# Performance work log

Hardware: AMD Instinct MI355X
Metric: run time of the kernel (lower is better)

## Reference

```python
import jax, jax.numpy as jnp
import numpy as np

NS = 16384   # N*S support examples
NQ = 16384   # N*Q query examples
D = 64       # embedding dim
N_CLASSES = 64


def setup_inputs() -> dict:
    key = jax.random.key(0)
    k1, k2, k3 = jax.random.split(key, 3)
    support_embeddings = jax.random.normal(k1, (NS, D), dtype=jnp.float32)
    query_embeddings = jax.random.normal(k2, (NQ, D), dtype=jnp.float32)
    labels = jax.random.randint(k3, (NS,), 0, N_CLASSES)
    support_labels_onehot = jax.nn.one_hot(labels, N_CLASSES, dtype=jnp.float32)
    return {
        "support_embeddings": support_embeddings,
        "query_embeddings": query_embeddings,
        "support_labels_onehot": support_labels_onehot,
    }


def reference(support_embeddings, query_embeddings, support_labels_onehot):
    # Pairwise L2 distance via ||q||^2 + ||s||^2 - 2 q.s (same math as
    # tf.norm(q[:,None,:] - s[None,:,:], axis=2) without the [NQ,NS,D] blowup).
    sq_s = jnp.sum(support_embeddings * support_embeddings, axis=-1)  # [NS]
    sq_q = jnp.sum(query_embeddings * query_embeddings, axis=-1)      # [NQ]
    cross = jnp.einsum('qd,sd->qs', query_embeddings, support_embeddings)  # [NQ,NS]
    d2 = sq_q[:, None] + sq_s[None, :] - 2.0 * cross
    distance = jnp.sqrt(jnp.maximum(d2, 0.0))
    # top_k(-distance, k=1) == first argmin along support axis
    indices = jnp.argmin(distance, axis=1)                 # [NQ]
    labels_x = jnp.argmax(support_labels_onehot, axis=1)   # [NS]
    labels_pred = labels_x[indices]                        # [NQ] gather
    num_classes = support_labels_onehot.shape[1]
    labels_prob = jax.nn.one_hot(labels_pred, num_classes, dtype=support_labels_onehot.dtype)
    return labels_prob
```

## Files before the change

kernel.cpp:

```cpp
#include <hip/hip_runtime.h>


#define NTOT   16384
#define DIM    64
#define EPS_COEF 0.004f
#define EPS_ABS  0.05f
#define CINIT_COEF (-0.499f)
#define FLT_BIG 3.4e38f

typedef __attribute__((ext_vector_type(8))) short short8;
typedef __attribute__((ext_vector_type(4))) float float4v;

__device__ __forceinline__ ushort f16_bits(float x) {
  union { _Float16 f; ushort u; } c;
  c.f = (_Float16)x;
  return c.u;
}

__device__ __forceinline__ void pin8(short8& v) {
  asm volatile("" : "+v"(v));
}

__global__ __launch_bounds__(256) void k_prep(
    const float* __restrict__ S, const float* __restrict__ Q,
    ushort* __restrict__ Sh, ushort* __restrict__ Qh,
    float* __restrict__ sqS, float* __restrict__ sqQ,
    float* __restrict__ sqSc, float* __restrict__ S_T) {
  __shared__ float tile[64][65];
  const int tid = threadIdx.x;
  const bool isS = blockIdx.x < 256;
  const int rbase = (blockIdx.x & 255) * 64;
  const float* __restrict__ src = isS ? S : Q;
  ushort* __restrict__ dh = isS ? Sh : Qh;

  const int tx = tid & 63;
  const int ty = tid >> 6;
#pragma unroll
  for (int i = 0; i < 16; ++i) {
    const int r = i * 4 + ty;
    tile[r][tx] = src[(size_t)(rbase + r) * DIM + tx];
  }
  __syncthreads();

  if (isS) {
#pragma unroll
    for (int i = 0; i < 16; ++i) {
      const int d = i * 4 + ty;
      S_T[(size_t)d * NTOT + rbase + tx] = tile[tx][d];
    }
  }

  const int panel = tid >> 6;
  const int half = (tid >> 5) & 1;
  const int slot0 = (tid & 31) * 2;
#pragma unroll
  for (int ss = 0; ss < 2; ++ss) {
    const int s = slot0 + ss;
    const int m = s & 15;
    const int q8 = s >> 4;
    const int row = panel * 16 + m;
    const int kb = half * 32 + q8 * 8;
    short8 hv;
#pragma unroll
    for (int j = 0; j < 8; ++j) hv[j] = (short)f16_bits(tile[row][kb + j]);
    const size_t goff =
        (size_t)((rbase >> 4) + panel) * 1024 + (size_t)half * 512 + (size_t)s * 8;
    *(short8*)&dh[goff] = hv;
  }

  if (tid < 64) {
    float acc = 0.0f;
#pragma unroll
    for (int d = 0; d < DIM; ++d) {
      const float v = tile[tid][d];
      acc = fmaf(v, v, acc);
    }
    if (isS) {
      sqS[rbase + tid] = acc;
      sqSc[rbase + tid] = CINIT_COEF * acc;
    } else {
      sqQ[rbase + tid] = acc;
    }
  }
}


#define MFMA16F(A, B, C) __builtin_amdgcn_mfma_f32_16x16x32_f16(A, B, C, 0, 0, 0)

template <int BST>
__global__ __launch_bounds__(256, 4) void k_phaseA(
    const ushort* __restrict__ Sh, const ushort* __restrict__ Qh,
    const float* __restrict__ sqSc, float* __restrict__ bmin) {
  constexpr int NSB = NTOT / (16 * BST);
  constexpr int SBLK = 16 * BST;
  __shared__ ushort spanel[2][4096];
  __shared__ float ssq[2][64];

  const int tid = threadIdx.x;
  const int l = tid & 63;
  const int w = tid >> 6;
  const int lm = l & 15;
  const int lq = l >> 4;
  const int split = blockIdx.x;
  const int qbase = blockIdx.y * 256 + w * 64;
  const int sbase = split * 512;

  short8 qh[4][2];
#pragma unroll
  for (int t = 0; t < 4; ++t) {
    const size_t pb = (size_t)((qbase >> 4) + t) * 1024 + (size_t)l * 8;
    qh[t][0] = *(const short8*)&Qh[pb];
    qh[t][1] = *(const short8*)&Qh[pb + 512];
  }
#pragma unroll
  for (int t = 0; t < 4; ++t) {
    pin8(qh[t][0]);
    pin8(qh[t][1]);
  }

  auto stage = [&](int c, int b) {
    const ushort* gs = Sh + ((size_t)(split * 32 + c * 4)) * 1024 +
                       (size_t)w * 1024 + (size_t)l * 8;
    ushort* ls = &spanel[b][w * 1024];
    __builtin_amdgcn_global_load_lds(
        (const __attribute__((address_space(1))) void*)(const void*)gs,
        (__attribute__((address_space(3))) void*)(void*)ls, 16, 0, 0);
    __builtin_amdgcn_global_load_lds(
        (const __attribute__((address_space(1))) void*)(const void*)(gs + 512),
        (__attribute__((address_space(3))) void*)(void*)(ls + 512), 16, 0, 0);
    if (tid < 16)
      *(float4*)&ssq[b][tid * 4] =
          *(const float4*)&sqSc[sbase + c * 64 + tid * 4];
  };

  float bmr[4] = {-FLT_BIG, -FLT_BIG, -FLT_BIG, -FLT_BIG};

  stage(0, 0);
  __syncthreads();

  for (int c = 0; c < 8; ++c) {
    const int b = c & 1;
    if (c + 1 < 8) stage(c + 1, b ^ 1);

#pragma unroll
    for (int st = 0; st < 4; ++st) {
      const short8 h0 = *(const short8*)&spanel[b][st * 1024 + l * 8];
      const short8 h1 = *(const short8*)&spanel[b][st * 1024 + 512 + l * 8];
      const float4 sqv = *(const float4*)&ssq[b][st * 16 + lq * 4];
      float4v cinit;
      cinit[0] = sqv.x;
      cinit[1] = sqv.y;
      cinit[2] = sqv.z;
      cinit[3] = sqv.w;
#pragma unroll
      for (int t = 0; t < 4; ++t) {
        float4v a = MFMA16F(h0, qh[t][0], cinit);
        a = MFMA16F(h1, qh[t][1], a);
        bmr[t] = fmaxf(fmaxf(fmaxf(a[0], a[1]), a[2]), fmaxf(a[3], bmr[t]));
      }
    }

    if ((((c + 1) * 4) & (BST - 1)) == 0) {
      const int gb = split * (512 / SBLK) + ((c + 1) * 64 / SBLK) - 1;
#pragma unroll
      for (int t = 0; t < 4; ++t) {
        float v = bmr[t];
        v = fmaxf(v, __shfl_xor(v, 16, 64));
        v = fmaxf(v, __shfl_xor(v, 32, 64));
        if (lq == 0) bmin[(size_t)(qbase + t * 16 + lm) * NSB + gb] = -2.0f * v;
        bmr[t] = -FLT_BIG;
      }
    }
    __syncthreads();
  }
}

template <int SBLK>
__global__ __launch_bounds__(256, 3) void k_phaseB(
    const float* __restrict__ S_T,
    const float* __restrict__ Q,
    const float* __restrict__ sqS, const float* __restrict__ sqQ,
    const float* __restrict__ bmin,
    const float* __restrict__ onehot, float* __restrict__ out) {
  constexpr int NSB = NTOT / SBLK;
  constexpr int NB64 = NSB / 64;
  constexpr int SPL = SBLK / 64;

  __shared__ float sQrow[4][64];
  __shared__ unsigned long long smask[4][NB64];
  __shared__ float sbk[4][4];
  __shared__ int sbi[4][4];

  const int lane = threadIdx.x & 63;
  const int w = threadIdx.x >> 6;
  const int q = blockIdx.x * 4 + w;

  if (lane < 16)
    *(float4*)&sQrow[w][lane * 4] = *(const float4*)&Q[(size_t)q * DIM + lane * 4];

  const float eps = EPS_COEF * sqQ[q] + EPS_ABS;

  float bv[NB64];
#pragma unroll
  for (int j = 0; j < NB64; ++j) bv[j] = bmin[(size_t)q * NSB + j * 64 + lane];
  float m = bv[0];
#pragma unroll
  for (int j = 1; j < NB64; ++j) m = fminf(m, bv[j]);
#pragma unroll
  for (int d = 1; d < 64; d <<= 1) m = fminf(m, __shfl_xor(m, d, 64));
  const float thr = m + eps;

#pragma unroll
  for (int j = 0; j < NB64; ++j) {
    const unsigned long long msk = __ballot(bv[j] <= thr);
    if (lane == 0) smask[w][j] = msk;
  }
  __syncthreads();

  int idx = 0;
  for (int qq = 0; qq < 4; ++qq) {
    float bkq = FLT_BIG;
    int biq = 0;
    for (int j = 0; j < NB64; ++j) {
      unsigned long long msk = smask[qq][j];
      while (msk) {
        const int b = j * 64 + (__ffsll((long long)msk) - 1);
        msk &= msk - 1;
        if ((idx++ & 3) != w) continue;
        const int s0 = b * SBLK + lane * SPL;
        if (SPL == 2) {
          float a0 = 0.f, a1 = 0.f;
#pragma unroll
          for (int h = 0; h < 2; ++h) {
            float2 x[32];
#pragma unroll
            for (int d = 0; d < 32; ++d)
              x[d] = *(const float2*)&S_T[(size_t)(h * 32 + d) * NTOT + s0];
#pragma unroll
            for (int d = 0; d < 32; ++d) {
              const float qd = sQrow[qq][h * 32 + d];
              a0 = fmaf(qd, x[d].x, a0);
              a1 = fmaf(qd, x[d].y, a1);
            }
          }
          const float2 sq2 = *(const float2*)&sqS[s0];
          const float k0 = fmaf(-2.f, a0, sq2.x);
          const float k1 = fmaf(-2.f, a1, sq2.y);
          bool u;
          u = k0 < bkq; bkq = u ? k0 : bkq; biq = u ? s0 : biq;
          u = k1 < bkq; bkq = u ? k1 : bkq; biq = u ? (s0 + 1) : biq;
        } else {
          float a0 = 0.f, a1 = 0.f, a2 = 0.f, a3 = 0.f;
#pragma unroll
          for (int hh = 0; hh < 4; ++hh) {
            float4 x[16];
#pragma unroll
            for (int d = 0; d < 16; ++d)
              x[d] = *(const float4*)&S_T[(size_t)(hh * 16 + d) * NTOT + s0];
#pragma unroll
            for (int d = 0; d < 16; ++d) {
              const float qd = sQrow[qq][hh * 16 + d];
              a0 = fmaf(qd, x[d].x, a0);
              a1 = fmaf(qd, x[d].y, a1);
              a2 = fmaf(qd, x[d].z, a2);
              a3 = fmaf(qd, x[d].w, a3);
            }
          }
          const float4 sq4 = *(const float4*)&sqS[s0];
          const float k0 = fmaf(-2.f, a0, sq4.x);
          const float k1 = fmaf(-2.f, a1, sq4.y);
          const float k2 = fmaf(-2.f, a2, sq4.z);
          const float k3 = fmaf(-2.f, a3, sq4.w);
          bool u;
          u = k0 < bkq; bkq = u ? k0 : bkq; biq = u ? s0 : biq;
          u = k1 < bkq; bkq = u ? k1 : bkq; biq = u ? (s0 + 1) : biq;
          u = k2 < bkq; bkq = u ? k2 : bkq; biq = u ? (s0 + 2) : biq;
          u = k3 < bkq; bkq = u ? k3 : bkq; biq = u ? (s0 + 3) : biq;
        }
      }
    }
#pragma unroll
    for (int d = 1; d < 64; d <<= 1) {
      const float ok = __shfl_xor(bkq, d, 64);
      const int oi = __shfl_xor(biq, d, 64);
      const bool u = (ok < bkq) || (ok == bkq && oi < biq);
      bkq = u ? ok : bkq;
      biq = u ? oi : biq;
    }
    if (lane == 0) { sbk[qq][w] = bkq; sbi[qq][w] = biq; }
  }
  __syncthreads();

  float fk = sbk[w][0];
  int fi = sbi[w][0];
#pragma unroll
  for (int ww = 1; ww < 4; ++ww) {
    const float ok = sbk[w][ww];
    const int oi = sbi[w][ww];
    const bool u = (ok < fk) || (ok == fk && oi < fi);
    fk = u ? ok : fk;
    fi = u ? oi : fi;
  }

  const float ov = onehot[(size_t)fi * 64 + lane];
  const unsigned long long lmask = __ballot(ov > 0.5f);
  const int label = __ffsll((long long)lmask) - 1;
  out[(size_t)q * 64 + lane] = (lane == label) ? 1.0f : 0.0f;
}

extern "C" void kernel_launch(void* const* d_in, const int* in_sizes, int n_in,
                              void* d_out, int out_size, void* d_ws, size_t ws_size,
                              hipStream_t stream) {
  const float* S = (const float*)d_in[0];
  const float* Q = (const float*)d_in[1];
  const float* OH = (const float*)d_in[2];
  float* out = (float*)d_out;

  char* ws = (char*)d_ws;
  ushort* Sh = (ushort*)ws;
  ushort* Qh = (ushort*)(ws + (2u << 20));
  float* S_T = (float*)(ws + (4u << 20));
  float* sqS = (float*)(ws + (8u << 20));
  float* sqQ = (float*)(ws + (8u << 20) + (64u << 10));
  float* sqSc = (float*)(ws + (8u << 20) + (128u << 10));
  float* bmin = (float*)(ws + (8u << 20) + (192u << 10));

  k_prep<<<dim3(512), 256, 0, stream>>>(S, Q, Sh, Qh, sqS, sqQ, sqSc, S_T);

  if (ws_size >= (17u << 20)) {
    k_phaseA<8><<<dim3(32, NTOT / 256), 256, 0, stream>>>(Sh, Qh, sqSc, bmin);
    k_phaseB<128><<<dim3(NTOT / 4), 256, 0, stream>>>(S_T, Q, sqS, sqQ,
                                                      bmin, OH, out);
  } else {
    k_phaseA<16><<<dim3(32, NTOT / 256), 256, 0, stream>>>(Sh, Qh, sqSc, bmin);
    k_phaseB<256><<<dim3(NTOT / 4), 256, 0, stream>>>(S_T, Q, sqS, sqQ,
                                                      bmin, OH, out);
  }
  (void)in_sizes; (void)n_in; (void)out_size; (void)ws_size;
}
```

Measured before the change: 145.8 us.

## Fuse prep kernel into phase A; convert and norm support rows on the fly

Removes the separate prep kernel. Phase A now loads fp32 support rows straight into LDS with an XOR swizzle, computes their squared norms and converts them to fp16 in-register, and converts query rows itself. Phase B reads row-major S instead of a transposed copy and recomputes the query norm locally. This saves a launch and the intermediate fp16/transpose buffers. In exchange it doubles the LDS traffic per support chunk, repeats the conversion and norm work in every query block, and gives phase B a non-coalesced row-strided gather.

```diff
diff --git a/kernel.cpp b/kernel.cpp
--- a/kernel.cpp
+++ b/kernel.cpp
@@ -21,80 +21,15 @@
   asm volatile("" : "+v"(v));
 }
 
-__global__ __launch_bounds__(256) void k_prep(
-    const float* __restrict__ S, const float* __restrict__ Q,
-    ushort* __restrict__ Sh, ushort* __restrict__ Qh,
-    float* __restrict__ sqS, float* __restrict__ sqQ,
-    float* __restrict__ sqSc, float* __restrict__ S_T) {
-  __shared__ float tile[64][65];
-  const int tid = threadIdx.x;
-  const bool isS = blockIdx.x < 256;
-  const int rbase = (blockIdx.x & 255) * 64;
-  const float* __restrict__ src = isS ? S : Q;
-  ushort* __restrict__ dh = isS ? Sh : Qh;
-
-  const int tx = tid & 63;
-  const int ty = tid >> 6;
-#pragma unroll
-  for (int i = 0; i < 16; ++i) {
-    const int r = i * 4 + ty;
-    tile[r][tx] = src[(size_t)(rbase + r) * DIM + tx];
-  }
-  __syncthreads();
-
-  if (isS) {
-#pragma unroll
-    for (int i = 0; i < 16; ++i) {
-      const int d = i * 4 + ty;
-      S_T[(size_t)d * NTOT + rbase + tx] = tile[tx][d];
-    }
-  }
-
-  const int panel = tid >> 6;
-  const int half = (tid >> 5) & 1;
-  const int slot0 = (tid & 31) * 2;
-#pragma unroll
-  for (int ss = 0; ss < 2; ++ss) {
-    const int s = slot0 + ss;
-    const int m = s & 15;
-    const int q8 = s >> 4;
-    const int row = panel * 16 + m;
-    const int kb = half * 32 + q8 * 8;
-    short8 hv;
-#pragma unroll
-    for (int j = 0; j < 8; ++j) hv[j] = (short)f16_bits(tile[row][kb + j]);
-    const size_t goff =
-        (size_t)((rbase >> 4) + panel) * 1024 + (size_t)half * 512 + (size_t)s * 8;
-    *(short8*)&dh[goff] = hv;
-  }
-
-  if (tid < 64) {
-    float acc = 0.0f;
-#pragma unroll
-    for (int d = 0; d < DIM; ++d) {
-      const float v = tile[tid][d];
-      acc = fmaf(v, v, acc);
-    }
-    if (isS) {
-      sqS[rbase + tid] = acc;
-      sqSc[rbase + tid] = CINIT_COEF * acc;
-    } else {
-      sqQ[rbase + tid] = acc;
-    }
-  }
-}
-
-
 #define MFMA16F(A, B, C) __builtin_amdgcn_mfma_f32_16x16x32_f16(A, B, C, 0, 0, 0)
 
 template <int BST>
 __global__ __launch_bounds__(256, 4) void k_phaseA(
-    const ushort* __restrict__ Sh, const ushort* __restrict__ Qh,
-    const float* __restrict__ sqSc, float* __restrict__ bmin) {
+    const float* __restrict__ S, const float* __restrict__ Q,
+    float* __restrict__ sqS, float* __restrict__ bmin) {
   constexpr int NSB = NTOT / (16 * BST);
   constexpr int SBLK = 16 * BST;
-  __shared__ ushort spanel[2][4096];
-  __shared__ float ssq[2][64];
+  __shared__ float schunk[2][4096];
 
   const int tid = threadIdx.x;
   const int l = tid & 63;
@@ -104,34 +39,44 @@
   const int split = blockIdx.x;
   const int qbase = blockIdx.y * 256 + w * 64;
   const int sbase = split * 512;
+  const bool writeSq = (blockIdx.y == 0);
 
   short8 qh[4][2];
 #pragma unroll
   for (int t = 0; t < 4; ++t) {
-    const size_t pb = (size_t)((qbase >> 4) + t) * 1024 + (size_t)l * 8;
-    qh[t][0] = *(const short8*)&Qh[pb];
-    qh[t][1] = *(const short8*)&Qh[pb + 512];
-  }
-#pragma unroll
-  for (int t = 0; t < 4; ++t) {
-    pin8(qh[t][0]);
-    pin8(qh[t][1]);
-  }
+    const float* qp = Q + (size_t)(qbase + t * 16 + lm) * 64 + lq * 8;
+#pragma unroll
+    for (int h = 0; h < 2; ++h) {
+      const float4 a = *(const float4*)(qp + h * 32);
+      const float4 b = *(const float4*)(qp + h * 32 + 4);
+      short8 v;
+      v[0] = (short)f16_bits(a.x); v[1] = (short)f16_bits(a.y);
+      v[2] = (short)f16_bits(a.z); v[3] = (short)f16_bits(a.w);
+      v[4] = (short)f16_bits(b.x); v[5] = (short)f16_bits(b.y);
+      v[6] = (short)f16_bits(b.z); v[7] = (short)f16_bits(b.w);
+      qh[t][h] = v;
+    }
+  }
+#pragma unroll
+  for (int t = 0; t < 4; ++t) { pin8(qh[t][0]); pin8(qh[t][1]); }
 
   auto stage = [&](int c, int b) {
-    const ushort* gs = Sh + ((size_t)(split * 32 + c * 4)) * 1024 +
-                       (size_t)w * 1024 + (size_t)l * 8;
-    ushort* ls = &spanel[b][w * 1024];
-    __builtin_amdgcn_global_load_lds(
-        (const __attribute__((address_space(1))) void*)(const void*)gs,
-        (__attribute__((address_space(3))) void*)(void*)ls, 16, 0, 0);
-    __builtin_amdgcn_global_load_lds(
-        (const __attribute__((address_space(1))) void*)(const void*)(gs + 512),
-        (__attribute__((address_space(3))) void*)(void*)(ls + 512), 16, 0, 0);
-    if (tid < 16)
-      *(float4*)&ssq[b][tid * 4] =
-          *(const float4*)&sqSc[sbase + c * 64 + tid * 4];
+    const size_t cb = (size_t)(sbase + c * 64) * 64;
+#pragma unroll
+    for (int I = 0; I < 4; ++I) {
+      const int r = w * 16 + I * 4 + (l >> 4);
+      const int dbl_ = lm ^ (r & 7);
+      const float* gs = S + cb + (size_t)r * 64 + dbl_ * 4;
+      float* ls = &schunk[b][w * 1024 + I * 256];
+      __builtin_amdgcn_global_load_lds(
+          (const __attribute__((address_space(1))) void*)(const void*)gs,
+          (__attribute__((address_space(3))) void*)(void*)ls, 16, 0, 0);
+    }
   };
+
+  const int xb = (l & 7) << 4;
+  const int o0f = ((lq * 32) ^ xb) >> 2;
+  const int o1f = (((lq * 32) + 16) ^ xb) >> 2;
 
   float bmr[4] = {-FLT_BIG, -FLT_BIG, -FLT_BIG, -FLT_BIG};
 
@@ -144,14 +89,40 @@
 
 #pragma unroll
     for (int st = 0; st < 4; ++st) {
-      const short8 h0 = *(const short8*)&spanel[b][st * 1024 + l * 8];
-      const short8 h1 = *(const short8*)&spanel[b][st * 1024 + 512 + l * 8];
-      const float4 sqv = *(const float4*)&ssq[b][st * 16 + lq * 4];
+      const float* sp = &schunk[b][(st * 16 + lm) * 64];
+      const float4 x0a = *(const float4*)(sp + o0f);
+      const float4 x0b = *(const float4*)(sp + o1f);
+      const float4 x1a = *(const float4*)(sp + o0f + 32);
+      const float4 x1b = *(const float4*)(sp + o1f + 32);
+
+      float p = 0.f;
+      p = fmaf(x0a.x, x0a.x, p); p = fmaf(x0a.y, x0a.y, p);
+      p = fmaf(x0a.z, x0a.z, p); p = fmaf(x0a.w, x0a.w, p);
+      p = fmaf(x0b.x, x0b.x, p); p = fmaf(x0b.y, x0b.y, p);
+      p = fmaf(x0b.z, x0b.z, p); p = fmaf(x0b.w, x0b.w, p);
+      p = fmaf(x1a.x, x1a.x, p); p = fmaf(x1a.y, x1a.y, p);
+      p = fmaf(x1a.z, x1a.z, p); p = fmaf(x1a.w, x1a.w, p);
+      p = fmaf(x1b.x, x1b.x, p); p = fmaf(x1b.y, x1b.y, p);
+      p = fmaf(x1b.z, x1b.z, p); p = fmaf(x1b.w, x1b.w, p);
+      p += __shfl_xor(p, 16, 64);
+      p += __shfl_xor(p, 32, 64);
+      if (writeSq && lq == 0) sqS[sbase + c * 64 + st * 16 + lm] = p;
+
       float4v cinit;
-      cinit[0] = sqv.x;
-      cinit[1] = sqv.y;
-      cinit[2] = sqv.z;
-      cinit[3] = sqv.w;
+#pragma unroll
+      for (int i = 0; i < 4; ++i)
+        cinit[i] = CINIT_COEF * __shfl(p, lq * 4 + i, 64);
+
+      short8 h0, h1;
+      h0[0] = (short)f16_bits(x0a.x); h0[1] = (short)f16_bits(x0a.y);
+      h0[2] = (short)f16_bits(x0a.z); h0[3] = (short)f16_bits(x0a.w);
+      h0[4] = (short)f16_bits(x0b.x); h0[5] = (short)f16_bits(x0b.y);
+      h0[6] = (short)f16_bits(x0b.z); h0[7] = (short)f16_bits(x0b.w);
+      h1[0] = (short)f16_bits(x1a.x); h1[1] = (short)f16_bits(x1a.y);
+      h1[2] = (short)f16_bits(x1a.z); h1[3] = (short)f16_bits(x1a.w);
+      h1[4] = (short)f16_bits(x1b.x); h1[5] = (short)f16_bits(x1b.y);
+      h1[6] = (short)f16_bits(x1b.z); h1[7] = (short)f16_bits(x1b.w);
+
 #pragma unroll
       for (int t = 0; t < 4; ++t) {
         float4v a = MFMA16F(h0, qh[t][0], cinit);
@@ -177,9 +148,9 @@
 
 template <int SBLK>
 __global__ __launch_bounds__(256, 3) void k_phaseB(
-    const float* __restrict__ S_T,
+    const float* __restrict__ S,
     const float* __restrict__ Q,
-    const float* __restrict__ sqS, const float* __restrict__ sqQ,
+    const float* __restrict__ sqS,
     const float* __restrict__ bmin,
     const float* __restrict__ onehot, float* __restrict__ out) {
   constexpr int NSB = NTOT / SBLK;
@@ -198,7 +169,13 @@
   if (lane < 16)
     *(float4*)&sQrow[w][lane * 4] = *(const float4*)&Q[(size_t)q * DIM + lane * 4];
 
-  const float eps = EPS_COEF * sqQ[q] + EPS_ABS;
+  float sqq = 0.f;
+#pragma unroll
+  for (int d = 0; d < 64; ++d) {
+    const float v = sQrow[w][d];
+    sqq = fmaf(v, v, sqq);
+  }
+  const float eps = EPS_COEF * sqq + EPS_ABS;
 
   float bv[NB64];
 #pragma unroll
@@ -228,19 +205,29 @@
         msk &= msk - 1;
         if ((idx++ & 3) != w) continue;
         const int s0 = b * SBLK + lane * SPL;
+        const float* rp = S + (size_t)s0 * 64;
         if (SPL == 2) {
           float a0 = 0.f, a1 = 0.f;
 #pragma unroll
           for (int h = 0; h < 2; ++h) {
-            float2 x[32];
-#pragma unroll
-            for (int d = 0; d < 32; ++d)
-              x[d] = *(const float2*)&S_T[(size_t)(h * 32 + d) * NTOT + s0];
-#pragma unroll
-            for (int d = 0; d < 32; ++d) {
-              const float qd = sQrow[qq][h * 32 + d];
-              a0 = fmaf(qd, x[d].x, a0);
-              a1 = fmaf(qd, x[d].y, a1);
+            float4 x0[8], x1[8];
+#pragma unroll
+            for (int j2 = 0; j2 < 8; ++j2)
+              x0[j2] = *(const float4*)(rp + h * 32 + j2 * 4);
+#pragma unroll
+            for (int j2 = 0; j2 < 8; ++j2)
+              x1[j2] = *(const float4*)(rp + 64 + h * 32 + j2 * 4);
+#pragma unroll
+            for (int j2 = 0; j2 < 8; ++j2) {
+              const int d = h * 32 + j2 * 4;
+              a0 = fmaf(sQrow[qq][d + 0], x0[j2].x, a0);
+              a1 = fmaf(sQrow[qq][d + 0], x1[j2].x, a1);
+              a0 = fmaf(sQrow[qq][d + 1], x0[j2].y, a0);
+              a1 = fmaf(sQrow[qq][d + 1], x1[j2].y, a1);
+              a0 = fmaf(sQrow[qq][d + 2], x0[j2].z, a0);
+              a1 = fmaf(sQrow[qq][d + 2], x1[j2].z, a1);
+              a0 = fmaf(sQrow[qq][d + 3], x0[j2].w, a0);
+              a1 = fmaf(sQrow[qq][d + 3], x1[j2].w, a1);
             }
           }
           const float2 sq2 = *(const float2*)&sqS[s0];
@@ -252,18 +239,26 @@
         } else {
           float a0 = 0.f, a1 = 0.f, a2 = 0.f, a3 = 0.f;
 #pragma unroll
-          for (int hh = 0; hh < 4; ++hh) {
-            float4 x[16];
-#pragma unroll
-            for (int d = 0; d < 16; ++d)
-              x[d] = *(const float4*)&S_T[(size_t)(hh * 16 + d) * NTOT + s0];
-#pragma unroll
-            for (int d = 0; d < 16; ++d) {
-              const float qd = sQrow[qq][hh * 16 + d];
-              a0 = fmaf(qd, x[d].x, a0);
-              a1 = fmaf(qd, x[d].y, a1);
-              a2 = fmaf(qd, x[d].z, a2);
-              a3 = fmaf(qd, x[d].w, a3);
+          for (int h = 0; h < 4; ++h) {
+            float4 x0[4], x1[4], x2[4], x3[4];
+#pragma unroll
+            for (int j2 = 0; j2 < 4; ++j2) {
+              x0[j2] = *(const float4*)(rp + h * 16 + j2 * 4);
+              x1[j2] = *(const float4*)(rp + 64 + h * 16 + j2 * 4);
+              x2[j2] = *(const float4*)(rp + 128 + h * 16 + j2 * 4);
+              x3[j2] = *(const float4*)(rp + 192 + h * 16 + j2 * 4);
+            }
+#pragma unroll
+            for (int j2 = 0; j2 < 4; ++j2) {
+              const int d = h * 16 + j2 * 4;
+#pragma unroll
+              for (int e = 0; e < 4; ++e) {
+                const float qd = sQrow[qq][d + e];
+                a0 = fmaf(qd, x0[j2][e], a0);
+                a1 = fmaf(qd, x1[j2][e], a1);
+                a2 = fmaf(qd, x2[j2][e], a2);
+                a3 = fmaf(qd, x3[j2][e], a3);
+              }
             }
           }
           const float4 sq4 = *(const float4*)&sqS[s0];
@@ -317,24 +312,16 @@
   float* out = (float*)d_out;
 
   char* ws = (char*)d_ws;
-  ushort* Sh = (ushort*)ws;
-  ushort* Qh = (ushort*)(ws + (2u << 20));
-  float* S_T = (float*)(ws + (4u << 20));
-  float* sqS = (float*)(ws + (8u << 20));
-  float* sqQ = (float*)(ws + (8u << 20) + (64u << 10));
-  float* sqSc = (float*)(ws + (8u << 20) + (128u << 10));
-  float* bmin = (float*)(ws + (8u << 20) + (192u << 10));
-
-  k_prep<<<dim3(512), 256, 0, stream>>>(S, Q, Sh, Qh, sqS, sqQ, sqSc, S_T);
-
-  if (ws_size >= (17u << 20)) {
-    k_phaseA<8><<<dim3(32, NTOT / 256), 256, 0, stream>>>(Sh, Qh, sqSc, bmin);
-    k_phaseB<128><<<dim3(NTOT / 4), 256, 0, stream>>>(S_T, Q, sqS, sqQ,
-                                                      bmin, OH, out);
+  float* bmin = (float*)ws;
+
+  if (ws_size >= (9u << 20)) {
+    float* sqS = (float*)(ws + (8u << 20));
+    k_phaseA<8><<<dim3(32, NTOT / 256), 256, 0, stream>>>(S, Q, sqS, bmin);
+    k_phaseB<128><<<dim3(NTOT / 4), 256, 0, stream>>>(S, Q, sqS, bmin, OH, out);
   } else {
-    k_phaseA<16><<<dim3(32, NTOT / 256), 256, 0, stream>>>(Sh, Qh, sqSc, bmin);
-    k_phaseB<256><<<dim3(NTOT / 4), 256, 0, stream>>>(S_T, Q, sqS, sqQ,
-                                                      bmin, OH, out);
+    float* sqS = (float*)(ws + (4u << 20));
+    k_phaseA<16><<<dim3(32, NTOT / 256), 256, 0, stream>>>(S, Q, sqS, bmin);
+    k_phaseB<256><<<dim3(NTOT / 4), 256, 0, stream>>>(S, Q, sqS, bmin, OH, out);
   }
   (void)in_sizes; (void)n_in; (void)out_size; (void)ws_size;
 }
```

Measured after the change: 221.7 us. +52.1%, slower.

## Deepen phaseA staging to 4-buffer pipeline and transpose bmin layout

Applied to the files above, without the earlier changes.

PhaseA now stages S panels three chunks ahead into a 4-deep LDS ring, using explicit vmcnt waits and raw s_barrier in place of a double buffer with full __syncthreads. The squared-norm constants for the whole 512-row split are loaded once up front instead of per chunk. The bmin intermediate is stored block-major (gb*NTOT + q) so phaseA writes coalesce across queries, and phaseB's reads are changed to match. This costs more LDS per block, which may limit occupancy, and the hand-written waitcnt counts rely on exactly two outstanding loads per stage.

```diff
diff --git a/kernel.cpp b/kernel.cpp
--- a/kernel.cpp
+++ b/kernel.cpp
@@ -20,6 +20,8 @@
 __device__ __forceinline__ void pin8(short8& v) {
   asm volatile("" : "+v"(v));
 }
+
+#define MFMA16F(A, B, C) __builtin_amdgcn_mfma_f32_16x16x32_f16(A, B, C, 0, 0, 0)
 
 __global__ __launch_bounds__(256) void k_prep(
     const float* __restrict__ S, const float* __restrict__ Q,
@@ -84,17 +86,13 @@
   }
 }
 
-
-#define MFMA16F(A, B, C) __builtin_amdgcn_mfma_f32_16x16x32_f16(A, B, C, 0, 0, 0)
-
 template <int BST>
 __global__ __launch_bounds__(256, 4) void k_phaseA(
     const ushort* __restrict__ Sh, const ushort* __restrict__ Qh,
     const float* __restrict__ sqSc, float* __restrict__ bmin) {
-  constexpr int NSB = NTOT / (16 * BST);
   constexpr int SBLK = 16 * BST;
-  __shared__ ushort spanel[2][4096];
-  __shared__ float ssq[2][64];
+  __shared__ ushort spanel[4][4096];
+  __shared__ float ssqAll[512];
 
   const int tid = threadIdx.x;
   const int l = tid & 63;
@@ -118,35 +116,42 @@
     pin8(qh[t][1]);
   }
 
-  auto stage = [&](int c, int b) {
+  {
+    const float2 v = *(const float2*)&sqSc[sbase + tid * 2];
+    *(float2*)&ssqAll[tid * 2] = v;
+  }
+
+  auto stage = [&](int c) {
     const ushort* gs = Sh + ((size_t)(split * 32 + c * 4)) * 1024 +
                        (size_t)w * 1024 + (size_t)l * 8;
-    ushort* ls = &spanel[b][w * 1024];
+    ushort* ls = &spanel[c & 3][w * 1024];
     __builtin_amdgcn_global_load_lds(
         (const __attribute__((address_space(1))) void*)(const void*)gs,
         (__attribute__((address_space(3))) void*)(void*)ls, 16, 0, 0);
     __builtin_amdgcn_global_load_lds(
         (const __attribute__((address_space(1))) void*)(const void*)(gs + 512),
         (__attribute__((address_space(3))) void*)(void*)(ls + 512), 16, 0, 0);
-    if (tid < 16)
-      *(float4*)&ssq[b][tid * 4] =
-          *(const float4*)&sqSc[sbase + c * 64 + tid * 4];
   };
 
   float bmr[4] = {-FLT_BIG, -FLT_BIG, -FLT_BIG, -FLT_BIG};
 
-  stage(0, 0);
-  __syncthreads();
-
+  stage(0);
+  stage(1);
+  stage(2);
+  asm volatile("s_waitcnt vmcnt(4) lgkmcnt(0)" ::: "memory");
+  __builtin_amdgcn_s_barrier();
+  __builtin_amdgcn_sched_barrier(0);
+
+#pragma unroll
   for (int c = 0; c < 8; ++c) {
-    const int b = c & 1;
-    if (c + 1 < 8) stage(c + 1, b ^ 1);
-
+    if (c + 3 < 8) stage(c + 3);
+
+    const int b = c & 3;
 #pragma unroll
     for (int st = 0; st < 4; ++st) {
       const short8 h0 = *(const short8*)&spanel[b][st * 1024 + l * 8];
       const short8 h1 = *(const short8*)&spanel[b][st * 1024 + 512 + l * 8];
-      const float4 sqv = *(const float4*)&ssq[b][st * 16 + lq * 4];
+      const float4 sqv = *(const float4*)&ssqAll[c * 64 + st * 16 + lq * 4];
       float4v cinit;
       cinit[0] = sqv.x;
       cinit[1] = sqv.y;
@@ -167,11 +172,23 @@
         float v = bmr[t];
         v = fmaxf(v, __shfl_xor(v, 16, 64));
         v = fmaxf(v, __shfl_xor(v, 32, 64));
-        if (lq == 0) bmin[(size_t)(qbase + t * 16 + lm) * NSB + gb] = -2.0f * v;
+        if (lq == 0)
+          bmin[(size_t)gb * NTOT + qbase + t * 16 + lm] = -2.0f * v;
         bmr[t] = -FLT_BIG;
       }
     }
-    __syncthreads();
+
+    if (c < 7) {
+      if (c < 5) {
+        asm volatile("s_waitcnt vmcnt(4)" ::: "memory");
+      } else if (c == 5) {
+        asm volatile("s_waitcnt vmcnt(2)" ::: "memory");
+      } else {
+        asm volatile("s_waitcnt vmcnt(0)" ::: "memory");
+      }
+      __builtin_amdgcn_s_barrier();
+      __builtin_amdgcn_sched_barrier(0);
+    }
   }
 }
 
@@ -202,7 +219,8 @@
 
   float bv[NB64];
 #pragma unroll
-  for (int j = 0; j < NB64; ++j) bv[j] = bmin[(size_t)q * NSB + j * 64 + lane];
+  for (int j = 0; j < NB64; ++j)
+    bv[j] = bmin[(size_t)(j * 64 + lane) * NTOT + q];
   float m = bv[0];
 #pragma unroll
   for (int j = 1; j < NB64; ++j) m = fminf(m, bv[j]);
```

After: 197.7 us. 1.36x slower.
